# Kernel tuning notes

Hardware: AMD Instinct MI355X
Metric: run time of the kernel (lower is better)

The kernel has to match this reference:

```python
import jax, jax.numpy as jnp
import numpy as np

# cfg constants (match init_kwargs)
K_CFG = 32
SPOT_K = 16
K_NN = max(K_CFG + 1, SPOT_K)  # = 33
DOWN_K = 8
SIGMA_C = 3.0
SEED_NUM = 128
SEED_THRESHOLD = 0.5

B, N, M, NC, MC = 1, 4096, 4096, 512, 512
CF, CC, H = 256, 1024, 256


def pairwise_sqdist(x, y):
    # x:(B,n,3) y:(B,m,3) -> (B,n,m) squared euclidean distance
    xx = jnp.sum(x * x, -1, keepdims=True)          # (B,n,1)
    yy = jnp.sum(y * y, -1, keepdims=True)          # (B,m,1)
    return xx - 2.0 * jnp.einsum('bnd,bmd->bnm', x, y) + jnp.swapaxes(yy, 1, 2)


def knn_idx(d, k):
    # smallest-k indices along last dim
    return jax.lax.top_k(-d, k)[1]


def compatibility(ref_d, src_d, mi):
    # ref_d:(B,N,N) src_d:(B,M,M) mi:(B,N) int -> (B,N) mean compatibility
    g = jnp.take_along_axis(src_d, mi[:, :, None], axis=1)   # (B,N,M) rows gathered
    g = jnp.take_along_axis(g, mi[:, None, :], axis=2)       # (B,N,N) cols gathered
    return jnp.mean(jax.nn.relu(1.0 - jnp.abs(ref_d - g) / SIGMA_C), axis=-1)


def seeding(compat, conf):
    # faithful to torch: selection = compat < max(compat)*threshold, weighted by confidence
    # jit-friendly fixed-size topk (seed_num) instead of data-dependent max_num
    sel = (compat < compat.max(-1, keepdims=True) * SEED_THRESHOLD).astype(conf.dtype)
    return jax.lax.top_k(sel * conf, SEED_NUM)[1]            # (B,SEED_NUM)


def setup_inputs() -> dict:
    key = jax.random.key(0)
    ks = jax.random.split(key, 12)
    inp = {
        'ref_points': jax.random.normal(ks[0], (B, N, 3), jnp.float32),
        'src_points': jax.random.normal(ks[1], (B, M, 3), jnp.float32),
        'ref_feats': jax.random.normal(ks[2], (B, N, CF), jnp.float32),
        'src_feats': jax.random.normal(ks[3], (B, M, CF), jnp.float32),
        'ref_points_c': jax.random.normal(ks[4], (B, NC, 3), jnp.float32),
        'src_points_c': jax.random.normal(ks[5], (B, MC, 3), jnp.float32),
        'ref_feats_c': jax.random.normal(ks[6], (B, NC, CC), jnp.float32),
        'src_feats_c': jax.random.normal(ks[7], (B, MC, CC), jnp.float32),
        'W1': jax.random.normal(ks[8], (CC, H), jnp.float32) / np.sqrt(CC),
        'b1': jnp.zeros((H,), jnp.float32),
        'W2': jax.random.normal(ks[9], (CF, H), jnp.float32) / np.sqrt(CF),
        'b2': jnp.zeros((H,), jnp.float32),
    }
    return inp


def reference(ref_points, src_points, ref_feats, src_feats,
              ref_points_c, src_points_c, ref_feats_c, src_feats_c,
              W1, b1, W2, b2):
    # --- KNN neighbor search (torch.no_grad block) ---
    ref_dists = pairwise_sqdist(ref_points, ref_points)     # (B,N,N)
    src_dists = pairwise_sqdist(src_points, src_points)     # (B,M,M)
    ref_idx = knn_idx(ref_dists, K_NN)                      # (B,N,K_NN)
    src_idx = knn_idx(src_dists, K_NN)
    ref_idx_up = knn_idx(pairwise_sqdist(ref_points, ref_points_c), 1)[..., 0]   # (B,N)
    src_idx_up = knn_idx(pairwise_sqdist(src_points, src_points_c), 1)[..., 0]
    ref_idx_down = knn_idx(pairwise_sqdist(ref_points_c, ref_points), DOWN_K)    # (B,NC,DOWN_K)
    src_idx_down = knn_idx(pairwise_sqdist(src_points_c, src_points), DOWN_K)

    # --- input projections ---
    hf_ref = ref_feats @ W2 + b2                            # (B,N,H)
    hf_src = src_feats @ W2 + b2
    hc_ref = ref_feats_c @ W1 + b1                          # (B,NC,H)
    hc_src = src_feats_c @ W1 + b1

    # --- dual-softmax matching scores ---
    scores = jnp.einsum('bnc,bmc->bnm', hf_ref, hf_src)     # (B,N,M)
    scores = jax.nn.softmax(scores, axis=-1) * jax.nn.softmax(scores, axis=-2)

    # --- ref -> src direction ---
    conf_r = jnp.max(scores, axis=-1)                       # (B,N)
    mi_r = jnp.argmax(scores, axis=-1)                      # (B,N)
    compat_r = compatibility(ref_dists, src_dists, mi_r)    # (B,N)
    seed_r = seeding(compat_r, conf_r * compat_r)           # (B,SEED_NUM)
    spot_r = jnp.take_along_axis(src_idx[..., :SPOT_K], mi_r[:, :, None], axis=1)  # (B,N,SPOT_K)

    # --- src -> ref direction ---
    scores_t = jnp.swapaxes(scores, 1, 2)
    conf_s = jnp.max(scores_t, axis=-1)
    mi_s = jnp.argmax(scores_t, axis=-1)
    compat_s = compatibility(src_dists, ref_dists, mi_s)
    seed_s = seeding(compat_s, conf_s * compat_s)
    spot_s = jnp.take_along_axis(ref_idx[..., :SPOT_K], mi_s[:, :, None], axis=1)

    return (scores, compat_r, compat_s, seed_r, seed_s, spot_r, spot_s,
            hc_ref, hc_src, ref_idx_up, src_idx_up, ref_idx_down, src_idx_down)
```

## Files before the change

### kernel.cpp

```cpp
#include <hip/hip_runtime.h>
#include <math.h>

#define NP 4096
#define NCP 512
#define HD 256
#define CCD 1024
#define SPOTK 16
#define DOWNK 8
#define SEEDN 128
#define JCH 512
#define NJC (NP / JCH)

__global__ __launch_bounds__(256) void gemm128_bt(
    const float* __restrict__ A, const float* __restrict__ B,
    float* __restrict__ C,
    float* __restrict__ pmaxR, float* __restrict__ psumR,
    float* __restrict__ pmaxC, float* __restrict__ psumC,
    int M, int N, int K)
{
    const int PAD = 132;
    __shared__ float As[16 * 132];
    __shared__ float Bs[16 * 132];

    const int bm = blockIdx.y * 128, bn = blockIdx.x * 128;
    const int t = threadIdx.x;
    const int tx = t & 15, ty = t >> 4;

    float acc[2][2][4][4] = {};

    const int rowA0 = t >> 2, kcA0 = (t & 3) * 4;
    const int rowA1 = (t + 256) >> 2, kcA1 = ((t + 256) & 3) * 4;

    float4 pa0 = *(const float4*)&A[(size_t)(bm + rowA0) * K + kcA0];
    float4 pa1 = *(const float4*)&A[(size_t)(bm + rowA1) * K + kcA1];
    float4 pb0 = *(const float4*)&B[(size_t)(bn + rowA0) * K + kcA0];
    float4 pb1 = *(const float4*)&B[(size_t)(bn + rowA1) * K + kcA1];

    for (int k0 = 0; k0 < K; k0 += 16) {
        As[(kcA0 + 0) * PAD + rowA0] = pa0.x;
        As[(kcA0 + 1) * PAD + rowA0] = pa0.y;
        As[(kcA0 + 2) * PAD + rowA0] = pa0.z;
        As[(kcA0 + 3) * PAD + rowA0] = pa0.w;
        As[(kcA1 + 0) * PAD + rowA1] = pa1.x;
        As[(kcA1 + 1) * PAD + rowA1] = pa1.y;
        As[(kcA1 + 2) * PAD + rowA1] = pa1.z;
        As[(kcA1 + 3) * PAD + rowA1] = pa1.w;
        Bs[(kcA0 + 0) * PAD + rowA0] = pb0.x;
        Bs[(kcA0 + 1) * PAD + rowA0] = pb0.y;
        Bs[(kcA0 + 2) * PAD + rowA0] = pb0.z;
        Bs[(kcA0 + 3) * PAD + rowA0] = pb0.w;
        Bs[(kcA1 + 0) * PAD + rowA1] = pb1.x;
        Bs[(kcA1 + 1) * PAD + rowA1] = pb1.y;
        Bs[(kcA1 + 2) * PAD + rowA1] = pb1.z;
        Bs[(kcA1 + 3) * PAD + rowA1] = pb1.w;
        __syncthreads();

        if (k0 + 16 < K) {
            int kn = k0 + 16;
            pa0 = *(const float4*)&A[(size_t)(bm + rowA0) * K + kn + kcA0];
            pa1 = *(const float4*)&A[(size_t)(bm + rowA1) * K + kn + kcA1];
            pb0 = *(const float4*)&B[(size_t)(bn + rowA0) * K + kn + kcA0];
            pb1 = *(const float4*)&B[(size_t)(bn + rowA1) * K + kn + kcA1];
        }

#pragma unroll
        for (int kk = 0; kk < 16; kk++) {
            float4 a0 = *(const float4*)&As[kk * PAD + ty * 4];
            float4 a1 = *(const float4*)&As[kk * PAD + ty * 4 + 64];
            float4 b0 = *(const float4*)&Bs[kk * PAD + tx * 4];
            float4 b1 = *(const float4*)&Bs[kk * PAD + tx * 4 + 64];
            float ar[2][4] = {{a0.x, a0.y, a0.z, a0.w}, {a1.x, a1.y, a1.z, a1.w}};
            float br[2][4] = {{b0.x, b0.y, b0.z, b0.w}, {b1.x, b1.y, b1.z, b1.w}};
#pragma unroll
            for (int qr = 0; qr < 2; qr++)
#pragma unroll
                for (int qc = 0; qc < 2; qc++)
#pragma unroll
                    for (int i = 0; i < 4; i++)
#pragma unroll
                        for (int j = 0; j < 4; j++)
                            acc[qr][qc][i][j] = fmaf(ar[qr][i], br[qc][j], acc[qr][qc][i][j]);
        }
        __syncthreads();
    }

#pragma unroll
    for (int qr = 0; qr < 2; qr++)
#pragma unroll
        for (int i = 0; i < 4; i++) {
            int m = bm + qr * 64 + ty * 4 + i;
#pragma unroll
            for (int qc = 0; qc < 2; qc++) {
                int n = bn + qc * 64 + tx * 4;
                float4 v = make_float4(acc[qr][qc][i][0], acc[qr][qc][i][1],
                                       acc[qr][qc][i][2], acc[qr][qc][i][3]);
                *(float4*)&C[(size_t)m * N + n] = v;
            }
        }

#pragma unroll
    for (int qr = 0; qr < 2; qr++)
#pragma unroll
        for (int i = 0; i < 4; i++) {
            float m = -INFINITY;
#pragma unroll
            for (int qc = 0; qc < 2; qc++)
#pragma unroll
                for (int j = 0; j < 4; j++) m = fmaxf(m, acc[qr][qc][i][j]);
            float s = 0.f;
#pragma unroll
            for (int qc = 0; qc < 2; qc++)
#pragma unroll
                for (int j = 0; j < 4; j++) s += expf(acc[qr][qc][i][j] - m);
#pragma unroll
            for (int off = 1; off < 16; off <<= 1) {
                float om = __shfl_xor(m, off), os = __shfl_xor(s, off);
                float Mx = fmaxf(m, om);
                s = s * expf(m - Mx) + os * expf(om - Mx);
                m = Mx;
            }
            if (tx == 0) {
                int r = bm + qr * 64 + ty * 4 + i;
                pmaxR[(size_t)blockIdx.x * NP + r] = m;
                psumR[(size_t)blockIdx.x * NP + r] = s;
            }
        }

    float* colm = As;
    float* cols_ = Bs;
#pragma unroll
    for (int qc = 0; qc < 2; qc++)
#pragma unroll
        for (int j = 0; j < 4; j++) {
            float m = -INFINITY;
#pragma unroll
            for (int qr = 0; qr < 2; qr++)
#pragma unroll
                for (int i = 0; i < 4; i++) m = fmaxf(m, acc[qr][qc][i][j]);
            float s = 0.f;
#pragma unroll
            for (int qr = 0; qr < 2; qr++)
#pragma unroll
                for (int i = 0; i < 4; i++) s += expf(acc[qr][qc][i][j] - m);
#pragma unroll
            for (int off = 16; off < 64; off <<= 1) {
                float om = __shfl_xor(m, off), os = __shfl_xor(s, off);
                float Mx = fmaxf(m, om);
                s = s * expf(m - Mx) + os * expf(om - Mx);
                m = Mx;
            }
            if ((ty & 3) == 0) {
                int w = ty >> 2, c = qc * 64 + tx * 4 + j;
                colm[w * 132 + c] = m;
                cols_[w * 132 + c] = s;
            }
        }
    __syncthreads();
    if (t < 128) {
        int c = t;
        float m = colm[c], s = cols_[c];
#pragma unroll
        for (int w = 1; w < 4; w++) {
            float om = colm[w * 132 + c], os = cols_[w * 132 + c];
            float Mx = fmaxf(m, om);
            s = s * expf(m - Mx) + os * expf(om - Mx);
            m = Mx;
        }
        pmaxC[(size_t)blockIdx.y * NP + bn + c] = m;
        psumC[(size_t)blockIdx.y * NP + bn + c] = s;
    }
}

__global__ __launch_bounds__(256) void combine_stats(const float* __restrict__ pmax,
                                                     const float* __restrict__ psum,
                                                     float* omax, float* osum)
{
    int m = blockIdx.x * 256 + threadIdx.x;
    float mx = -INFINITY;
    for (int c = 0; c < 32; c++) mx = fmaxf(mx, pmax[(size_t)c * NP + m]);
    float sum = 0.f;
    for (int c = 0; c < 32; c++) sum += psum[(size_t)c * NP + m] * expf(pmax[(size_t)c * NP + m] - mx);
    omax[m] = mx; osum[m] = sum;
}

__global__ __launch_bounds__(256) void gemm64(
    const float* __restrict__ A0, const float* __restrict__ A1,
    const float* __restrict__ B, const float* __restrict__ bias,
    float* __restrict__ C0, float* __restrict__ C1,
    int M, int N, int K)
{
    const float* A = blockIdx.z ? A1 : A0;
    float* C = blockIdx.z ? C1 : C0;

    const int PAD = 68;
    __shared__ float As[16 * 68];
    __shared__ float Bs[16 * 68];

    const int bm = blockIdx.y * 64, bn = blockIdx.x * 64;
    const int t = threadIdx.x;
    const int tx = t & 15, ty = t >> 4;

    float acc[4][4] = {};

    for (int k0 = 0; k0 < K; k0 += 16) {
        {
            int row = t >> 2, kc = (t & 3) * 4;
            float4 v = *(const float4*)&A[(size_t)(bm + row) * K + k0 + kc];
            As[(kc + 0) * PAD + row] = v.x;
            As[(kc + 1) * PAD + row] = v.y;
            As[(kc + 2) * PAD + row] = v.z;
            As[(kc + 3) * PAD + row] = v.w;
        }
        {
            int k = t >> 4, n4 = (t & 15) * 4;
            float4 v = *(const float4*)&B[(size_t)(k0 + k) * N + bn + n4];
            *(float4*)&Bs[k * PAD + n4] = v;
        }
        __syncthreads();
#pragma unroll
        for (int kk = 0; kk < 16; kk++) {
            float4 a4 = *(const float4*)&As[kk * PAD + ty * 4];
            float4 b4 = *(const float4*)&Bs[kk * PAD + tx * 4];
            float ar[4] = {a4.x, a4.y, a4.z, a4.w};
            float br[4] = {b4.x, b4.y, b4.z, b4.w};
#pragma unroll
            for (int i = 0; i < 4; i++)
#pragma unroll
                for (int j = 0; j < 4; j++)
                    acc[i][j] = fmaf(ar[i], br[j], acc[i][j]);
        }
        __syncthreads();
    }
    float4 b4 = *(const float4*)&bias[bn + tx * 4];
#pragma unroll
    for (int i = 0; i < 4; i++) {
        int m = bm + ty * 4 + i;
        float4 v = make_float4(acc[i][0] + b4.x, acc[i][1] + b4.y,
                               acc[i][2] + b4.z, acc[i][3] + b4.w);
        *(float4*)&C[(size_t)m * N + bn + tx * 4] = v;
    }
}

__global__ __launch_bounds__(256) void gemm64_atomic(
    const float* __restrict__ A0, const float* __restrict__ A1,
    const float* __restrict__ B,
    float* __restrict__ C0, float* __restrict__ C1,
    int M, int N, int K, int KCH)
{
    int pair = blockIdx.z >> 3, ks = blockIdx.z & 7;
    const float* A = pair ? A1 : A0;
    float* C = pair ? C1 : C0;

    const int PAD = 68;
    __shared__ float As[16 * 68];
    __shared__ float Bs[16 * 68];

    const int bm = blockIdx.y * 64, bn = blockIdx.x * 64;
    const int t = threadIdx.x;
    const int tx = t & 15, ty = t >> 4;
    const int kbeg = ks * KCH, kend = kbeg + KCH;

    float acc[4][4] = {};

    for (int k0 = kbeg; k0 < kend; k0 += 16) {
        {
            int row = t >> 2, kc = (t & 3) * 4;
            float4 v = *(const float4*)&A[(size_t)(bm + row) * K + k0 + kc];
            As[(kc + 0) * PAD + row] = v.x;
            As[(kc + 1) * PAD + row] = v.y;
            As[(kc + 2) * PAD + row] = v.z;
            As[(kc + 3) * PAD + row] = v.w;
        }
        {
            int k = t >> 4, n4 = (t & 15) * 4;
            float4 v = *(const float4*)&B[(size_t)(k0 + k) * N + bn + n4];
            *(float4*)&Bs[k * PAD + n4] = v;
        }
        __syncthreads();
#pragma unroll
        for (int kk = 0; kk < 16; kk++) {
            float4 a4 = *(const float4*)&As[kk * PAD + ty * 4];
            float4 b4 = *(const float4*)&Bs[kk * PAD + tx * 4];
            float ar[4] = {a4.x, a4.y, a4.z, a4.w};
            float br[4] = {b4.x, b4.y, b4.z, b4.w};
#pragma unroll
            for (int i = 0; i < 4; i++)
#pragma unroll
                for (int j = 0; j < 4; j++)
                    acc[i][j] = fmaf(ar[i], br[j], acc[i][j]);
        }
        __syncthreads();
    }
#pragma unroll
    for (int i = 0; i < 4; i++) {
        int m = bm + ty * 4 + i;
#pragma unroll
        for (int j = 0; j < 4; j++)
            atomicAdd(&C[(size_t)m * N + bn + tx * 4 + j], acc[i][j]);
    }
}

__global__ void init_hc(const float* __restrict__ b1,
                        float* __restrict__ o_hcr, float* __restrict__ o_hcs)
{
    int idx = blockIdx.x * 256 + threadIdx.x;
    float b = b1[idx & (HD - 1)];
    o_hcr[idx] = b; o_hcs[idx] = b;
}

__global__ void pack_pts(const float* __restrict__ p0, const float* __restrict__ p1,
                         const float* __restrict__ p2, const float* __restrict__ p3,
                         float4* o0, float4* o1, float4* o2, float4* o3)
{
    int z = blockIdx.z;
    const float* p = (z == 0) ? p0 : (z == 1) ? p1 : (z == 2) ? p2 : p3;
    float4* o      = (z == 0) ? o0 : (z == 1) ? o1 : (z == 2) ? o2 : o3;
    int n = (z < 2) ? NP : NCP;
    int i = blockIdx.x * 256 + threadIdx.x;
    if (i >= n) return;
    float x = p[i * 3], y = p[i * 3 + 1], zz = p[i * 3 + 2];
    o[i] = make_float4(x, y, zz, x * x + y * y + zz * zz);
}

__global__ __launch_bounds__(256) void finalize_rows(float* __restrict__ s,
    const float* __restrict__ rmax, const float* __restrict__ rsum,
    const float* __restrict__ cmax, const float* __restrict__ csum,
    float* __restrict__ confr, int* __restrict__ mir)
{
    int n = blockIdx.x;
    float rm = rmax[n], rs = rsum[n];
    size_t base = (size_t)n * NP;
    float best = -INFINITY; int bi = 0x7fffffff;
    for (int m1 = threadIdx.x; m1 < NP; m1 += 256) {
        float v = s[base + m1];
        float a = expf(v - rm) / rs;
        float b = expf(v - cmax[m1]) / csum[m1];
        float sc = a * b;
        s[base + m1] = sc;
        if (sc > best) { best = sc; bi = m1; }
    }
    __shared__ float rv[256]; __shared__ int ri[256];
    rv[threadIdx.x] = best; ri[threadIdx.x] = bi; __syncthreads();
    for (int off = 128; off; off >>= 1) {
        if (threadIdx.x < off) {
            float v2 = rv[threadIdx.x + off]; int i2 = ri[threadIdx.x + off];
            if (v2 > rv[threadIdx.x] || (v2 == rv[threadIdx.x] && i2 < ri[threadIdx.x])) {
                rv[threadIdx.x] = v2; ri[threadIdx.x] = i2;
            }
        }
        __syncthreads();
    }
    if (threadIdx.x == 0) { confr[n] = rv[0]; mir[n] = ri[0]; }
}

__global__ __launch_bounds__(256) void col_argmax_partial(const float* __restrict__ s,
                                                          float* pconf, int* pmi)
{
    int m = blockIdx.x * 256 + threadIdx.x;
    int n0 = blockIdx.y * 128;
    float best = -INFINITY; int bi = 0;
    for (int n = n0; n < n0 + 128; n++) {
        float v = s[(size_t)n * NP + m];
        if (v > best) { best = v; bi = n; }
    }
    pconf[(size_t)blockIdx.y * NP + m] = best;
    pmi[(size_t)blockIdx.y * NP + m] = bi;
}

__global__ __launch_bounds__(256) void col_argmax_combine(const float* __restrict__ pconf,
                                                          const int* __restrict__ pmi,
                                                          float* confs, int* mis)
{
    int m = blockIdx.x * 256 + threadIdx.x;
    float best = -INFINITY; int bi = 0;
    for (int c = 0; c < 32; c++) {
        float v = pconf[(size_t)c * NP + m];
        if (v > best) { best = v; bi = pmi[(size_t)c * NP + m]; }
    }
    confs[m] = best; mis[m] = bi;
}

__global__ void gather_pts(const float4* __restrict__ p4A, const float4* __restrict__ p4B,
                           const int* __restrict__ miA, const int* __restrict__ miB,
                           float4* __restrict__ qA, float4* __restrict__ qB)
{
    const float4* p4 = blockIdx.z ? p4B : p4A;
    const int*    mi = blockIdx.z ? miB : miA;
    float4*       q  = blockIdx.z ? qB : qA;
    int j = blockIdx.x * 256 + threadIdx.x;
    if (j >= NP) return;
    q[j] = p4[mi[j]];
}

__global__ __launch_bounds__(256) void compat_kernel(
    const float4* __restrict__ baseA, const float4* __restrict__ baseB,
    const float4* __restrict__ qA, const float4* __restrict__ qB,
    float* __restrict__ o1A, float* __restrict__ o1B,
    float* __restrict__ o2A, float* __restrict__ o2B)
{
    const float4* base = blockIdx.z ? baseB : baseA;
    const float4* q    = blockIdx.z ? qB : qA;
    float* out1        = blockIdx.z ? o1B : o1A;
    float* out2        = blockIdx.z ? o2B : o2A;
    int n = blockIdx.x;
    float4 b = base[n];
    float4 a = q[n];
    float sum = 0.f;
    for (int j = threadIdx.x; j < NP; j += 256) {
        float4 p = base[j];
        float rt = b.x * p.x + b.y * p.y + b.z * p.z;
        float rd = (b.w - 2.f * rt) + p.w;
        float4 qj = q[j];
        float st = a.x * qj.x + a.y * qj.y + a.z * qj.z;
        float sd = (a.w - 2.f * st) + qj.w;
        float c = 1.f - fabsf(rd - sd) / 3.0f;
        sum += fmaxf(c, 0.f);
    }
    __shared__ float red[256];
    red[threadIdx.x] = sum; __syncthreads();
    for (int off = 128; off; off >>= 1) {
        if (threadIdx.x < off) red[threadIdx.x] += red[threadIdx.x + off];
        __syncthreads();
    }
    if (threadIdx.x == 0) { float c = red[0] * (1.0f / NP); out1[n] = c; out2[n] = c; }
}

__global__ __launch_bounds__(256) void seed_prep(
    const float* __restrict__ compatA, const float* __restrict__ compatB,
    const float* __restrict__ confA, const float* __restrict__ confB,
    float* __restrict__ wA, float* __restrict__ wB)
{
    const float* compat = blockIdx.z ? compatB : compatA;
    const float* conf   = blockIdx.z ? confB : confA;
    float* w            = blockIdx.z ? wB : wA;
    __shared__ float red[256];
    int tid = threadIdx.x;
    float mx = -INFINITY;
    for (int j = tid; j < NP; j += 256) mx = fmaxf(mx, compat[j]);
    red[tid] = mx; __syncthreads();
    for (int off = 128; off; off >>= 1) {
        if (tid < off) red[tid] = fmaxf(red[tid], red[tid + off]);
        __syncthreads();
    }
    float thr = red[0] * 0.5f;
    for (int j = tid; j < NP; j += 256) {
        float c = compat[j];
        w[j] = (c < thr) ? conf[j] * c : 0.0f;
    }
}

__global__ __launch_bounds__(256) void seed_rank_partial(
    const float* __restrict__ wA, const float* __restrict__ wB,
    int* __restrict__ rankpA, int* __restrict__ rankpB)
{
    const float* w = blockIdx.z ? wB : wA;
    int* rankp     = blockIdx.z ? rankpB : rankpA;
    int tid = threadIdx.x;
    int jc = blockIdx.y;

    __shared__ float4 wj[JCH / 4];
    if (tid < JCH / 4) wj[tid] = ((const float4*)w)[jc * (JCH / 4) + tid];
    __syncthreads();

    int i = blockIdx.x * 256 + tid;
    float wi = w[i];
    int jbase = jc * JCH;
    int r0 = 0, r1 = 0, r2 = 0, r3 = 0;
#pragma unroll 4
    for (int j4 = 0; j4 < JCH / 4; j4++) {
        float4 v = wj[j4];
        int j = jbase + j4 * 4;
        r0 += (v.x > wi || (v.x == wi && (j    ) < i));
        r1 += (v.y > wi || (v.y == wi && (j + 1) < i));
        r2 += (v.z > wi || (v.z == wi && (j + 2) < i));
        r3 += (v.w > wi || (v.w == wi && (j + 3) < i));
    }
    rankp[(size_t)jc * NP + i] = (r0 + r1) + (r2 + r3);
}

__global__ __launch_bounds__(256) void seed_scatter(
    const int* __restrict__ rankpA, const int* __restrict__ rankpB,
    float* __restrict__ outA, float* __restrict__ outB)
{
    const int* rankp = blockIdx.z ? rankpB : rankpA;
    float* outp      = blockIdx.z ? outB : outA;
    int i = blockIdx.x * 256 + threadIdx.x;
    int r = 0;
#pragma unroll
    for (int jc = 0; jc < NJC; jc++) r += rankp[(size_t)jc * NP + i];
    if (r < SEEDN) outp[r] = (float)i;
}

__device__ __forceinline__ void bitonic64_val(float& d, int lane)
{
#pragma unroll
    for (int k = 2; k <= 64; k <<= 1)
#pragma unroll
        for (int j = k >> 1; j > 0; j >>= 1) {
            float od = __shfl_xor(d, j);
            bool lower = ((lane & j) == 0);
            bool asc   = ((lane & k) == 0);
            bool take = (lower == asc) ? (od < d) : (d < od);
            d = take ? od : d;
        }
}

__device__ __forceinline__ void bitonic64_lex(float& d, int& i, int lane)
{
#pragma unroll
    for (int k = 2; k <= 64; k <<= 1)
#pragma unroll
        for (int j = k >> 1; j > 0; j >>= 1) {
            float od = __shfl_xor(d, j);
            int   oi = __shfl_xor(i, j);
            bool lower = ((lane & j) == 0);
            bool asc   = ((lane & k) == 0);
            bool less = (od < d) || (od == d && oi < i);
            bool gtr  = (d < od) || (d == od && i < oi);
            bool take = (lower == asc) ? less : gtr;
            d = take ? od : d;
            i = take ? oi : i;
        }
}

template<int KSEL>
__device__ __forceinline__ void merge_chunk(float& run_d, int& run_i,
                                            float cd, int ci, int lane)
{
    bitonic64_lex(cd, ci, lane);
    int src = lane - KSEL;
    int s2 = (src >= 0 && src < KSEL) ? src : 0;
    float cd2 = __shfl(cd, s2);
    int   ci2 = __shfl(ci, s2);
    float nd = (lane < KSEL) ? run_d : ((lane < 2 * KSEL) ? cd2 : INFINITY);
    int   ni = (lane < KSEL) ? run_i : ((lane < 2 * KSEL) ? ci2 : 0x7fffffff);
    bitonic64_lex(nd, ni, lane);
    run_d = nd; run_i = ni;
}

template<int KSEL>
__global__ __launch_bounds__(256) void knn_topk(
    const float4* __restrict__ rowA, const float4* __restrict__ rowB,
    const float4* __restrict__ colA, const float4* __restrict__ colB,
    int ncols,
    int* __restrict__ outiA, int* __restrict__ outiB,
    float* __restrict__ outfA, float* __restrict__ outfB)
{
    const float4* rowp = blockIdx.z ? rowB : rowA;
    const float4* colp = blockIdx.z ? colB : colA;
    int* outi = blockIdx.z ? outiB : outiA;
    float* outf = blockIdx.z ? outfB : outfA;

    int wid = threadIdx.x >> 6, lane = threadIdx.x & 63;
    int r = blockIdx.x * 4 + wid;

    float4 p = rowp[r];

    float mn = INFINITY;
    for (int j0 = 0; j0 < ncols; j0 += 64) {
        float4 c = colp[j0 + lane];
        float t = p.x * c.x + p.y * c.y + p.z * c.z;
        float d = (p.w - 2.f * t) + c.w;
        mn = fminf(mn, d);
    }
    bitonic64_val(mn, lane);
    float T = __shfl(mn, KSEL - 1) + 1e-4f;

    __shared__ float qd[4][256];
    __shared__ int   qi[4][256];
    int cnt = 0; bool ovf = false;
    for (int j0 = 0; j0 < ncols; j0 += 64) {
        int j = j0 + lane;
        float4 c = colp[j];
        float t = p.x * c.x + p.y * c.y + p.z * c.z;
        float d = (p.w - 2.f * t) + c.w;
        bool keep = (d <= T);
        unsigned long long mask = __ballot(keep);
        int nsel = __popcll(mask);
        if (cnt + nsel > 256) { ovf = true; break; }
        if (keep) {
            int pos = cnt + (int)__popcll(mask & ((1ull << lane) - 1ull));
            qd[wid][pos] = d; qi[wid][pos] = j;
        }
        cnt += nsel;
    }

    float run_d = INFINITY; int run_i = 0x7fffffff;
    if (!ovf) {
        for (int c = 0; c < cnt; c += 64) {
            int idx = c + lane;
            float cd = (idx < cnt) ? qd[wid][idx] : INFINITY;
            int   ci = (idx < cnt) ? qi[wid][idx] : 0x7fffffff;
            merge_chunk<KSEL>(run_d, run_i, cd, ci, lane);
        }
    } else {
        for (int j0 = 0; j0 < ncols; j0 += 64) {
            int j = j0 + lane;
            float4 c = colp[j];
            float t = p.x * c.x + p.y * c.y + p.z * c.z;
            float d = (p.w - 2.f * t) + c.w;
            merge_chunk<KSEL>(run_d, run_i, d, j, lane);
        }
    }

    if (lane < KSEL) {
        if (outi) outi[(size_t)r * KSEL + lane] = run_i;
        else      outf[(size_t)r * KSEL + lane] = (float)run_i;
    }
}

__global__ __launch_bounds__(256) void up_argmin(
    const float4* __restrict__ ptsA, const float4* __restrict__ ptsB,
    const float4* __restrict__ ptscA, const float4* __restrict__ ptscB,
    float* __restrict__ outA, float* __restrict__ outB)
{
    const float4* pts   = blockIdx.z ? ptsB : ptsA;
    const float4* pts_c = blockIdx.z ? ptscB : ptscA;
    float* out_f        = blockIdx.z ? outB : outA;
    __shared__ float4 cp[NCP];
    for (int c = threadIdx.x; c < NCP; c += 256) cp[c] = pts_c[c];
    __syncthreads();
    int n = blockIdx.x * 256 + threadIdx.x;
    float4 p = pts[n];
    float best = INFINITY; int bi = 0;
    for (int c = 0; c < NCP; c++) {
        float4 q = cp[c];
        float t = p.x * q.x + p.y * q.y + p.z * q.z;
        float d = (p.w - 2.f * t) + q.w;
        if (d < best) { best = d; bi = c; }
    }
    out_f[n] = (float)bi;
}

__global__ void spot_gather(const int* __restrict__ idxA, const int* __restrict__ idxB,
                            const int* __restrict__ miA, const int* __restrict__ miB,
                            float* __restrict__ outA, float* __restrict__ outB)
{
    const int* idx16 = blockIdx.z ? idxB : idxA;
    const int* mi    = blockIdx.z ? miB : miA;
    float* outp      = blockIdx.z ? outB : outA;
    int t = blockIdx.x * 256 + threadIdx.x;
    int n = t >> 4, k = t & 15;
    outp[t] = (float)idx16[(size_t)mi[n] * SPOTK + k];
}

extern "C" void kernel_launch(void* const* d_in, const int* in_sizes, int n_in,
                              void* d_out, int out_size, void* d_ws, size_t ws_size,
                              hipStream_t stream)
{
    const float* ref_points   = (const float*)d_in[0];
    const float* src_points   = (const float*)d_in[1];
    const float* ref_feats    = (const float*)d_in[2];
    const float* src_feats    = (const float*)d_in[3];
    const float* ref_points_c = (const float*)d_in[4];
    const float* src_points_c = (const float*)d_in[5];
    const float* ref_feats_c  = (const float*)d_in[6];
    const float* src_feats_c  = (const float*)d_in[7];
    const float* W1 = (const float*)d_in[8];
    const float* b1 = (const float*)d_in[9];
    const float* W2 = (const float*)d_in[10];
    const float* b2 = (const float*)d_in[11];

    float* out = (float*)d_out;
    float* o_scores = out;
    float* o_compr  = o_scores + (size_t)NP * NP;
    float* o_comps  = o_compr + NP;
    float* o_seedr  = o_comps + NP;
    float* o_seeds  = o_seedr + SEEDN;
    float* o_spotr  = o_seeds + SEEDN;
    float* o_spots  = o_spotr + (size_t)NP * SPOTK;
    float* o_hcr    = o_spots + (size_t)NP * SPOTK;
    float* o_hcs    = o_hcr + (size_t)NCP * HD;
    float* o_rup    = o_hcs + (size_t)NCP * HD;
    float* o_sup    = o_rup + NP;
    float* o_rdown  = o_sup + NP;
    float* o_sdown  = o_rdown + (size_t)NCP * DOWNK;

    float* ws = (float*)d_ws;
    float* hfr   = ws;
    float* hfs   = hfr + (size_t)NP * HD;
    float* rmax  = hfs + (size_t)NP * HD;
    float* rsum  = rmax + NP;
    float* cmax  = rsum + NP;
    float* csum  = cmax + NP;
    float* confr = csum + NP;
    float* confs = confr + NP;
    float* compr = confs + NP;
    float* comps = compr + NP;
    int*   mir   = (int*)(comps + NP);
    int*   mis   = mir + NP;
    float* pmax  = (float*)(mis + NP);
    float* psum  = pmax + 32 * NP;
    float* pconf = psum + 32 * NP;
    int*   pmi   = (int*)(pconf + 32 * NP);
    float4* qr   = (float4*)(pmi + 32 * NP);
    float4* qs   = qr + NP;
    int* ridx16  = (int*)(qs + NP);
    int* sidx16  = ridx16 + (size_t)NP * SPOTK;
    float4* rp4  = (float4*)(sidx16 + (size_t)NP * SPOTK);
    float4* sp4  = rp4 + NP;
    float4* rcp4 = sp4 + NP;
    float4* scp4 = rcp4 + NCP;
    float* wA    = (float*)(scp4 + NCP);
    float* wB    = wA + NP;
    int* rankpA  = (int*)(wB + NP);
    int* rankpB  = rankpA + NJC * NP;
    size_t ws_need = (size_t)((float*)(rankpB + NJC * NP) - ws) * 4;
    if (ws_size < ws_need) return;

    float* pmaxR = pconf;
    float* psumR = (float*)pmi;

    dim3 b256(256);

    pack_pts<<<dim3(NP / 256, 1, 4), b256, 0, stream>>>(
        ref_points, src_points, ref_points_c, src_points_c, rp4, sp4, rcp4, scp4);

    init_hc<<<dim3((NCP * HD) / 256), b256, 0, stream>>>(b1, o_hcr, o_hcs);
    gemm64_atomic<<<dim3(HD / 64, NCP / 64, 16), b256, 0, stream>>>(
        ref_feats_c, src_feats_c, W1, o_hcr, o_hcs, NCP, HD, CCD, CCD / 8);

    gemm64<<<dim3(HD / 64, NP / 64, 2), b256, 0, stream>>>(
        ref_feats, src_feats, W2, b2, hfr, hfs, NP, HD, HD);

    gemm128_bt<<<dim3(32, 32, 1), b256, 0, stream>>>(
        hfr, hfs, o_scores, pmaxR, psumR, pmax, psum, NP, NP, HD);
    combine_stats<<<16, b256, 0, stream>>>(pmaxR, psumR, rmax, rsum);
    combine_stats<<<16, b256, 0, stream>>>(pmax, psum, cmax, csum);

    knn_topk<SPOTK><<<dim3(NP / 4, 1, 2), b256, 0, stream>>>(
        rp4, sp4, rp4, sp4, NP, ridx16, sidx16, nullptr, nullptr);
    knn_topk<DOWNK><<<dim3(NCP / 4, 1, 2), b256, 0, stream>>>(
        rcp4, scp4, rp4, sp4, NP, nullptr, nullptr, o_rdown, o_sdown);
    up_argmin<<<dim3(NP / 256, 1, 2), b256, 0, stream>>>(
        rp4, sp4, rcp4, scp4, o_rup, o_sup);

    finalize_rows<<<NP, b256, 0, stream>>>(o_scores, rmax, rsum, cmax, csum, confr, mir);
    col_argmax_partial<<<dim3(16, 32), b256, 0, stream>>>(o_scores, pconf, pmi);
    col_argmax_combine<<<16, b256, 0, stream>>>(pconf, pmi, confs, mis);

    gather_pts<<<dim3(NP / 256, 1, 2), b256, 0, stream>>>(
        sp4, rp4, mir, mis, qr, qs);
    compat_kernel<<<dim3(NP, 1, 2), b256, 0, stream>>>(
        rp4, sp4, qr, qs, o_compr, o_comps, compr, comps);

    seed_prep<<<dim3(1, 1, 2), b256, 0, stream>>>(
        compr, comps, confr, confs, wA, wB);
    seed_rank_partial<<<dim3(NP / 256, NJC, 2), b256, 0, stream>>>(
        wA, wB, rankpA, rankpB);
    seed_scatter<<<dim3(NP / 256, 1, 2), b256, 0, stream>>>(
        rankpA, rankpB, o_seedr, o_seeds);

    spot_gather<<<dim3((NP * SPOTK) / 256, 1, 2), b256, 0, stream>>>(
        sidx16, ridx16, mir, mis, o_spotr, o_spots);
}
```

Before: 521.5 us.

## Merge small launches and drop register prefetch in score GEMM tile loads

Merges the two combine_stats launches into one grid with a z dimension, and merges the point gather with the spot gather into a single four-slice kernel, cutting two kernel launches. The 128x128 score GEMM stops prefetching the next k-slice into registers and instead loads and stores each tile to shared memory inside the loop. That lowers register pressure but exposes global load latency before each barrier. The gather_spot grid launches many early-exit blocks for the two point-gather slices.

```diff
diff --git a/kernel.cpp b/kernel.cpp
--- a/kernel.cpp
+++ b/kernel.cpp
@@ -28,41 +28,23 @@
 
     float acc[2][2][4][4] = {};
 
-    const int rowA0 = t >> 2, kcA0 = (t & 3) * 4;
-    const int rowA1 = (t + 256) >> 2, kcA1 = ((t + 256) & 3) * 4;
-
-    float4 pa0 = *(const float4*)&A[(size_t)(bm + rowA0) * K + kcA0];
-    float4 pa1 = *(const float4*)&A[(size_t)(bm + rowA1) * K + kcA1];
-    float4 pb0 = *(const float4*)&B[(size_t)(bn + rowA0) * K + kcA0];
-    float4 pb1 = *(const float4*)&B[(size_t)(bn + rowA1) * K + kcA1];
-
     for (int k0 = 0; k0 < K; k0 += 16) {
-        As[(kcA0 + 0) * PAD + rowA0] = pa0.x;
-        As[(kcA0 + 1) * PAD + rowA0] = pa0.y;
-        As[(kcA0 + 2) * PAD + rowA0] = pa0.z;
-        As[(kcA0 + 3) * PAD + rowA0] = pa0.w;
-        As[(kcA1 + 0) * PAD + rowA1] = pa1.x;
-        As[(kcA1 + 1) * PAD + rowA1] = pa1.y;
-        As[(kcA1 + 2) * PAD + rowA1] = pa1.z;
-        As[(kcA1 + 3) * PAD + rowA1] = pa1.w;
-        Bs[(kcA0 + 0) * PAD + rowA0] = pb0.x;
-        Bs[(kcA0 + 1) * PAD + rowA0] = pb0.y;
-        Bs[(kcA0 + 2) * PAD + rowA0] = pb0.z;
-        Bs[(kcA0 + 3) * PAD + rowA0] = pb0.w;
-        Bs[(kcA1 + 0) * PAD + rowA1] = pb1.x;
-        Bs[(kcA1 + 1) * PAD + rowA1] = pb1.y;
-        Bs[(kcA1 + 2) * PAD + rowA1] = pb1.z;
-        Bs[(kcA1 + 3) * PAD + rowA1] = pb1.w;
-        __syncthreads();
-
-        if (k0 + 16 < K) {
-            int kn = k0 + 16;
-            pa0 = *(const float4*)&A[(size_t)(bm + rowA0) * K + kn + kcA0];
-            pa1 = *(const float4*)&A[(size_t)(bm + rowA1) * K + kn + kcA1];
-            pb0 = *(const float4*)&B[(size_t)(bn + rowA0) * K + kn + kcA0];
-            pb1 = *(const float4*)&B[(size_t)(bn + rowA1) * K + kn + kcA1];
-        }
-
+#pragma unroll
+        for (int it = 0; it < 2; it++) {
+            int idx = t + it * 256;
+            int row = idx >> 2, kc = (idx & 3) * 4;
+            float4 va = *(const float4*)&A[(size_t)(bm + row) * K + k0 + kc];
+            As[(kc + 0) * PAD + row] = va.x;
+            As[(kc + 1) * PAD + row] = va.y;
+            As[(kc + 2) * PAD + row] = va.z;
+            As[(kc + 3) * PAD + row] = va.w;
+            float4 vb = *(const float4*)&B[(size_t)(bn + row) * K + k0 + kc];
+            Bs[(kc + 0) * PAD + row] = vb.x;
+            Bs[(kc + 1) * PAD + row] = vb.y;
+            Bs[(kc + 2) * PAD + row] = vb.z;
+            Bs[(kc + 3) * PAD + row] = vb.w;
+        }
+        __syncthreads();
 #pragma unroll
         for (int kk = 0; kk < 16; kk++) {
             float4 a0 = *(const float4*)&As[kk * PAD + ty * 4];
@@ -171,10 +153,15 @@
     }
 }
 
-__global__ __launch_bounds__(256) void combine_stats(const float* __restrict__ pmax,
-                                                     const float* __restrict__ psum,
-                                                     float* omax, float* osum)
-{
+__global__ __launch_bounds__(256) void combine_stats(
+    const float* __restrict__ pmaxA, const float* __restrict__ psumA,
+    const float* __restrict__ pmaxB, const float* __restrict__ psumB,
+    float* omaxA, float* osumA, float* omaxB, float* osumB)
+{
+    const float* pmax = blockIdx.z ? pmaxB : pmaxA;
+    const float* psum = blockIdx.z ? psumB : psumA;
+    float* omax       = blockIdx.z ? omaxB : omaxA;
+    float* osum       = blockIdx.z ? osumB : osumA;
     int m = blockIdx.x * 256 + threadIdx.x;
     float mx = -INFINITY;
     for (int c = 0; c < 32; c++) mx = fmaxf(mx, pmax[(size_t)c * NP + m]);
@@ -380,16 +367,28 @@
     confs[m] = best; mis[m] = bi;
 }
 
-__global__ void gather_pts(const float4* __restrict__ p4A, const float4* __restrict__ p4B,
-                           const int* __restrict__ miA, const int* __restrict__ miB,
-                           float4* __restrict__ qA, float4* __restrict__ qB)
-{
-    const float4* p4 = blockIdx.z ? p4B : p4A;
-    const int*    mi = blockIdx.z ? miB : miA;
-    float4*       q  = blockIdx.z ? qB : qA;
-    int j = blockIdx.x * 256 + threadIdx.x;
-    if (j >= NP) return;
-    q[j] = p4[mi[j]];
+__global__ void gather_spot(
+    const float4* __restrict__ sp4, const float4* __restrict__ rp4,
+    const int* __restrict__ sidx16, const int* __restrict__ ridx16,
+    const int* __restrict__ mir, const int* __restrict__ mis,
+    float4* __restrict__ qr, float4* __restrict__ qs,
+    float* __restrict__ o_spotr, float* __restrict__ o_spots)
+{
+    int z = blockIdx.z;
+    int t = blockIdx.x * 256 + threadIdx.x;
+    if (z < 2) {
+        if (t >= NP) return;
+        const float4* p4 = z ? rp4 : sp4;
+        const int*    mi = z ? mis : mir;
+        float4*       q  = z ? qs : qr;
+        q[t] = p4[mi[t]];
+    } else {
+        int n = t >> 4, k = t & 15;
+        const int* idx16 = (z == 2) ? sidx16 : ridx16;
+        const int* mi    = (z == 2) ? mir : mis;
+        float* outp      = (z == 2) ? o_spotr : o_spots;
+        outp[t] = (float)idx16[(size_t)mi[n] * SPOTK + k];
+    }
 }
 
 __global__ __launch_bounds__(256) void compat_kernel(
@@ -630,18 +629,6 @@
         if (d < best) { best = d; bi = c; }
     }
     out_f[n] = (float)bi;
-}
-
-__global__ void spot_gather(const int* __restrict__ idxA, const int* __restrict__ idxB,
-                            const int* __restrict__ miA, const int* __restrict__ miB,
-                            float* __restrict__ outA, float* __restrict__ outB)
-{
-    const int* idx16 = blockIdx.z ? idxB : idxA;
-    const int* mi    = blockIdx.z ? miB : miA;
-    float* outp      = blockIdx.z ? outB : outA;
-    int t = blockIdx.x * 256 + threadIdx.x;
-    int n = t >> 4, k = t & 15;
-    outp[t] = (float)idx16[(size_t)mi[n] * SPOTK + k];
 }
 
 extern "C" void kernel_launch(void* const* d_in, const int* in_sizes, int n_in,
@@ -725,8 +712,8 @@
 
     gemm128_bt<<<dim3(32, 32, 1), b256, 0, stream>>>(
         hfr, hfs, o_scores, pmaxR, psumR, pmax, psum, NP, NP, HD);
-    combine_stats<<<16, b256, 0, stream>>>(pmaxR, psumR, rmax, rsum);
-    combine_stats<<<16, b256, 0, stream>>>(pmax, psum, cmax, csum);
+    combine_stats<<<dim3(16, 1, 2), b256, 0, stream>>>(
+        pmaxR, psumR, pmax, psum, rmax, rsum, cmax, csum);
 
     knn_topk<SPOTK><<<dim3(NP / 4, 1, 2), b256, 0, stream>>>(
         rp4, sp4, rp4, sp4, NP, ridx16, sidx16, nullptr, nullptr);
@@ -739,8 +726,9 @@
     col_argmax_partial<<<dim3(16, 32), b256, 0, stream>>>(o_scores, pconf, pmi);
     col_argmax_combine<<<16, b256, 0, stream>>>(pconf, pmi, confs, mis);
 
-    gather_pts<<<dim3(NP / 256, 1, 2), b256, 0, stream>>>(
-        sp4, rp4, mir, mis, qr, qs);
+    gather_spot<<<dim3((NP * SPOTK) / 256, 1, 4), b256, 0, stream>>>(
+        sp4, rp4, sidx16, ridx16, mir, mis, qr, qs, o_spotr, o_spots);
+
     compat_kernel<<<dim3(NP, 1, 2), b256, 0, stream>>>(
         rp4, sp4, qr, qs, o_compr, o_comps, compr, comps);
 
@@ -750,7 +738,4 @@
         wA, wB, rankpA, rankpB);
     seed_scatter<<<dim3(NP / 256, 1, 2), b256, 0, stream>>>(
         rankpA, rankpB, o_seedr, o_seeds);
-
-    spot_gather<<<dim3((NP * SPOTK) / 256, 1, 2), b256, 0, stream>>>(
-        sidx16, ridx16, mir, mis, o_spotr, o_spots);
-}
+}
```

Measured after the change: 523.9 us. Within noise of the previous version (+0.5%).
